# Optimization experiments

Measured on AMD Instinct MI355X. Metric: run time of the kernel, lower is better.

## Reference

```python
import jax, jax.numpy as jnp
import numpy as np
import math

B, S, E = 2, 2048, 1024
H = 16
D = E // H  # head dim = 64


def setup_inputs() -> dict:
    key = jax.random.key(0)
    ks = jax.random.split(key, 9)
    s = 1.0 / math.sqrt(E)
    return {
        "x": jax.random.normal(ks[0], (B, S, E), dtype=jnp.float32),
        "Wq": jax.random.uniform(ks[1], (E, E), jnp.float32, -s, s),
        "bq": jnp.zeros((E,), jnp.float32),
        "Wk": jax.random.uniform(ks[2], (E, E), jnp.float32, -s, s),
        "bk": jnp.zeros((E,), jnp.float32),
        "Wv": jax.random.uniform(ks[3], (E, E), jnp.float32, -s, s),
        "bv": jnp.zeros((E,), jnp.float32),
        "Wo": jax.random.uniform(ks[4], (E, E), jnp.float32, -s, s),
        "bo": jnp.zeros((E,), jnp.float32),
    }


def reference(x, Wq, bq, Wk, bk, Wv, bv, Wo, bo):
    b, s, e = x.shape
    q = x @ Wq + bq  # [B,S,E]
    k = x @ Wk + bk
    v = x @ Wv + bv
    # [B,S,E] -> [B,H,S,D]
    q = q.reshape(b, s, H, D).transpose(0, 2, 1, 3)
    k = k.reshape(b, s, H, D).transpose(0, 2, 1, 3)
    v = v.reshape(b, s, H, D).transpose(0, 2, 1, 3)
    scores = jnp.einsum('bhqd,bhkd->bhqk', q, k) / jnp.sqrt(jnp.float32(D))
    causal = jnp.tril(jnp.ones((s, s), dtype=bool))  # keep lower triangle
    scores = jnp.where(causal, scores, -jnp.inf)
    attn = jax.nn.softmax(scores, axis=-1)
    # dropout is identity in eval mode
    out = jnp.einsum('bhqk,bhkd->bhqd', attn, v)
    out = out.transpose(0, 2, 1, 3).reshape(b, s, e)
    return out @ Wo + bo
```

## Files before the change

kernel.cpp:

```cpp
#include <hip/hip_runtime.h>
#include <hip/hip_bf16.h>
#include <math.h>

#define B_ 2
#define S_ 2048
#define E_ 1024
#define H_ 16
#define D_ 64
#define M_ (B_*S_)

typedef __attribute__((ext_vector_type(8))) short short8v;
typedef __attribute__((ext_vector_type(4))) float floatx4;

__device__ __forceinline__ short f2bf(float f) {
    union { float f; unsigned u; } x; x.f = f;
    unsigned r = (x.u + 0x7fffu + ((x.u >> 16) & 1u)) >> 16;
    return (short)r;
}

__device__ __forceinline__ unsigned pk_bf16(float a, float b) {
    union { float f; unsigned u; } x, y;
    x.f = a; y.f = b;
    return __builtin_amdgcn_perm(y.u + 0x8000u, x.u + 0x8000u, 0x07060302u);
}

__device__ __forceinline__ float fast_exp2(float x) {
#if __has_builtin(__builtin_amdgcn_exp2f)
    return __builtin_amdgcn_exp2f(x);
#else
    return __expf(x * 0.6931471805599453f);
#endif
}

__device__ __forceinline__ void gl2lds16(const void* g, void* l) {
    __builtin_amdgcn_global_load_lds(
        (const __attribute__((address_space(1))) void*)g,
        (__attribute__((address_space(3))) void*)l, 16, 0, 0);
}

__device__ __forceinline__ int swz_off(int row, int cg) {
    return row*64 + (((cg ^ (row & 7)) & 7) << 3);
}

__global__ __launch_bounds__(256) void convert_x(
    const float* __restrict__ x, short* __restrict__ xb)
{
    const size_t i = ((size_t)blockIdx.x*256 + threadIdx.x) * 8;
    float4 a = *(const float4*)(x + i);
    float4 b = *(const float4*)(x + i + 4);
    int4 p = { (int)pk_bf16(a.x,a.y), (int)pk_bf16(a.z,a.w),
               (int)pk_bf16(b.x,b.y), (int)pk_bf16(b.z,b.w) };
    *(int4*)(xb + i) = p;
}

__global__ __launch_bounds__(256) void transpose_w(
    const float* __restrict__ W0, const float* __restrict__ W1,
    const float* __restrict__ W2, const float* __restrict__ W3,
    short* __restrict__ T0, short* __restrict__ T1,
    short* __restrict__ T2, short* __restrict__ T3)
{
    const int z = blockIdx.z;
    const float* W = (z==0)?W0:(z==1)?W1:(z==2)?W2:W3;
    short*       T = (z==0)?T0:(z==1)?T1:(z==2)?T2:T3;
    __shared__ float tile[32][33];
    const int k0 = blockIdx.y*32, n0 = blockIdx.x*32;
    const int r = threadIdx.x >> 5, c = threadIdx.x & 31;
    #pragma unroll
    for (int i=0;i<4;i++)
        tile[r+8*i][c] = W[(size_t)(k0+r+8*i)*E_ + n0 + c];
    __syncthreads();
    #pragma unroll
    for (int i=0;i<4;i++)
        T[(size_t)(n0+r+8*i)*E_ + k0 + c] = f2bf(tile[c][r+8*i]);
}

__global__ __launch_bounds__(512, 2) void qkv_gemm(
    const short* __restrict__ xb, const short* __restrict__ Wt,
    const float* __restrict__ bq, const float* __restrict__ bk, const float* __restrict__ bv,
    short* __restrict__ Qo, short* __restrict__ Ko, short* __restrict__ Vo)
{
    __shared__ __align__(16) short As[2][256*64];
    __shared__ __align__(16) short Bs[2][256*64];

    const int t = threadIdx.x;
    const int wave = t >> 6, lane = t & 63;
    const int quad = lane >> 4, l15 = lane & 15;
    const int wr = wave >> 2, wc = wave & 3;

    const int bid = blockIdx.x;
    const int sw  = (bid & 7) * 24 + (bid >> 3);
    const int m0  = (sw / 12) * 256;
    const int nti = sw % 12;
    const int nf0 = nti * 256;
    const int z   = nf0 >> 10;
    const float* bb = (z==0) ? bq : (z==1) ? bk : bv;
    short* out      = (z==0) ? Qo : (z==1) ? Ko : Vo;
    const float sc  = (z==0) ? 0.18033688011112042f : 1.0f;

    const int sr8 = lane >> 3;
    const int scs = ((lane & 7) ^ sr8) * 8;

    const short* Ag = xb + (size_t)m0  * E_;
    const short* Bg = Wt + (size_t)nf0 * E_;

    floatx4 acc[8][4];
    #pragma unroll
    for (int i=0;i<8;i++)
        #pragma unroll
        for (int j=0;j<4;j++) acc[i][j] = (floatx4){0.f,0.f,0.f,0.f};

    auto stageA = [&](int p, int h, int kt) {
        const int rb = h*128 + wave*16;
        const short* src = Ag + (size_t)(rb + sr8)*E_ + kt*64 + scs;
        #pragma unroll
        for (int c=0;c<2;c++)
            gl2lds16(src + (size_t)c*8*E_, &As[p][(rb + c*8)*64]);
    };
    auto stageB = [&](int p, int h, int kt) {
        const int rb = h*128 + wave*16;
        const short* src = Bg + (size_t)(rb + sr8)*E_ + kt*64 + scs;
        #pragma unroll
        for (int c=0;c<2;c++)
            gl2lds16(src + (size_t)c*8*E_, &Bs[p][(rb + c*8)*64]);
    };

    short8v a[4][2], b[4][2];
    auto rdA = [&](int p, int row16, int ks) -> short8v {
        return *(const short8v*)&As[p][swz_off(wr*128 + row16*16 + l15, quad + ks*4)];
    };
    auto rdB = [&](int p, int row16, int ks) -> short8v {
        return *(const short8v*)&Bs[p][swz_off(wc*64  + row16*16 + l15, quad + ks*4)];
    };
    auto mm = [&](int mbase, int nbase) {
        #pragma unroll
        for (int mt=0;mt<4;mt++)
            #pragma unroll
            for (int nt=0;nt<2;nt++)
                #pragma unroll
                for (int ks=0;ks<2;ks++)
                    acc[mbase+mt][nbase+nt] = __builtin_amdgcn_mfma_f32_16x16x32_bf16(
                        a[mt][ks], b[nbase+nt][ks], acc[mbase+mt][nbase+nt], 0,0,0);
    };

    auto ktile = [&](int tt, int p) {
        #pragma unroll
        for (int mt=0;mt<4;mt++){ a[mt][0]=rdA(p,mt,0); a[mt][1]=rdA(p,mt,1); }
        #pragma unroll
        for (int nt=0;nt<2;nt++){ b[nt][0]=rdB(p,nt,0); b[nt][1]=rdB(p,nt,1); }
        if (tt+1 < 16) stageA(p^1, 0, tt+1);
        __builtin_amdgcn_s_barrier();
        __builtin_amdgcn_s_setprio(1);
        mm(0,0);
        __builtin_amdgcn_s_setprio(0);
        __builtin_amdgcn_s_barrier();
        #pragma unroll
        for (int nt=2;nt<4;nt++){ b[nt][0]=rdB(p,nt,0); b[nt][1]=rdB(p,nt,1); }
        if (tt+1 < 16) stageA(p^1, 1, tt+1);
        __builtin_amdgcn_s_barrier();
        __builtin_amdgcn_s_setprio(1);
        mm(0,2);
        __builtin_amdgcn_s_setprio(0);
        __builtin_amdgcn_s_barrier();
        #pragma unroll
        for (int mt=0;mt<4;mt++){ a[mt][0]=rdA(p,4+mt,0); a[mt][1]=rdA(p,4+mt,1); }
        if (tt+2 < 16) stageB(p, 0, tt+2);
        __builtin_amdgcn_s_barrier();
        __builtin_amdgcn_s_setprio(1);
        mm(4,0);
        __builtin_amdgcn_s_setprio(0);
        __builtin_amdgcn_s_barrier();
        if (tt+2 < 16) stageB(p, 1, tt+2);
        __builtin_amdgcn_s_barrier();
        __builtin_amdgcn_s_setprio(1);
        mm(4,2);
        __builtin_amdgcn_s_setprio(0);
        if (tt+2 < 16)      asm volatile("s_waitcnt vmcnt(4)" ::: "memory");
        else if (tt+1 < 16) asm volatile("s_waitcnt vmcnt(0)" ::: "memory");
        __builtin_amdgcn_s_barrier();
    };

    stageA(0,0,0); stageA(0,1,0); stageB(0,0,0); stageB(0,1,0);
    stageB(1,0,1); stageB(1,1,1);
    asm volatile("s_waitcnt vmcnt(4)" ::: "memory");
    __builtin_amdgcn_s_barrier();

    #pragma unroll 1
    for (int tb = 0; tb < 16; tb += 2) {
        ktile(tb,   0);
        ktile(tb+1, 1);
    }

    #pragma unroll
    for (int nt=0;nt<4;nt++) {
        const int nw = (nf0 & 1023) + wc*64 + nt*16 + l15;
        const float bias = bb[nw];
        const int h = nw >> 6, d = nw & 63;
        #pragma unroll
        for (int mt=0;mt<8;mt++) {
            #pragma unroll
            for (int r=0;r<4;r++) {
                const int m = m0 + wr*128 + mt*16 + quad*4 + r;
                const int b2 = m >> 11, s = m & (S_-1);
                const int bh = (b2<<4) + h;
                const float v = (acc[mt][nt][r] + bias) * sc;
                if (z == 0) {
                    out[((size_t)bh*S_ + s)*D_ + d] = f2bf(v);
                } else if (z == 1) {
                    const int ts = s >> 6, kk = s & 63;
                    const int c = kk*8 + ((d>>3) ^ ((kk>>2)&7));
                    out[((size_t)bh*32 + ts)*4096 + c*8 + (d&7)] = f2bf(v);
                } else {
                    const int ts = s >> 6, sk = s & 63;
                    const int c = d*8 + ((sk>>3) ^ (d&7));
                    out[((size_t)bh*32 + ts)*4096 + c*8 + (sk&7)] = f2bf(v);
                }
            }
        }
    }
}

__global__ __launch_bounds__(256, 1) void attn_kernel(
    const short* __restrict__ Q, const short* __restrict__ K, const short* __restrict__ V,
    short* __restrict__ AO)
{
    const int bh = blockIdx.x;
    const int qb = (gridDim.y - 1 - blockIdx.y) * 128;
    const int t = threadIdx.x;
    const int wave = t >> 6, lane = t & 63;
    const int quad = lane >> 4, l15 = lane & 15;

    const short* Qp = Q + (size_t)bh * (S_*D_);
    const short* Kp = K + (size_t)bh * (S_*D_);
    const short* Vp = V + (size_t)bh * (S_*D_);

    __shared__ __align__(16) short KVs[2][8192];
    __shared__ __align__(16) short Psl[2][4][2][16*72];

    const int qA = qb + wave*16;
    const int qB = qb + 64 + wave*16;
    const short* qa = Qp + (size_t)(qA + l15)*D_ + quad*8;
    const short8v qA0 = *(const short8v*)qa, qA1 = *(const short8v*)(qa + 32);
    const short* qbp = Qp + (size_t)(qB + l15)*D_ + quad*8;
    const short8v qB0 = *(const short8v*)qbp, qB1 = *(const short8v*)(qbp + 32);

    const int qrbA = qA + quad*4;
    const int qrbB = qB + quad*4;

    floatx4 oA[4], oB[4];
    #pragma unroll
    for (int i=0;i<4;i++) { oA[i] = (floatx4){0,0,0,0}; oB[i] = (floatx4){0,0,0,0}; }
    float tsA[4] = {0,0,0,0}, tsB[4] = {0,0,0,0};

    const int L = (qb >> 6) + 2;
    const int swz = l15 & 7;

    auto stage = [&](int kt, int p) {
        const short* src = ((wave < 2) ? Kp : Vp) + (size_t)kt*4096 + (wave&1)*2048 + lane*8;
        short* dst = &KVs[p][((wave < 2) ? 0 : 4096) + (wave&1)*2048];
        #pragma unroll
        for (int c=0;c<4;c++)
            gl2lds16(src + c*512, dst + c*512);
    };
    auto qk2 = [&](const short* KL, floatx4 (&sA)[4], floatx4 (&sB)[4]) {
        #pragma unroll
        for (int h=0; h<4; h++) {
            const int rowc = (4*l15 + h)*8;
            short8v b0 = *(const short8v*)(KL + (rowc + (quad       ^ swz))*8);
            short8v b1 = *(const short8v*)(KL + (rowc + ((4 + quad) ^ swz))*8);
            sA[h] = (floatx4){0.f,0.f,0.f,0.f};
            sA[h] = __builtin_amdgcn_mfma_f32_16x16x32_bf16(qA0, b0, sA[h], 0,0,0);
            sA[h] = __builtin_amdgcn_mfma_f32_16x16x32_bf16(qA1, b1, sA[h], 0,0,0);
            sB[h] = (floatx4){0.f,0.f,0.f,0.f};
            sB[h] = __builtin_amdgcn_mfma_f32_16x16x32_bf16(qB0, b0, sB[h], 0,0,0);
            sB[h] = __builtin_amdgcn_mfma_f32_16x16x32_bf16(qB1, b1, sB[h], 0,0,0);
        }
    };
    auto soft_u = [&](floatx4 (&s)[4], float* ts, short* pw, int qrb, int k0) {
        const int kk = k0 + 4*l15;
        #pragma unroll
        for (int r=0; r<4; r++) {
            const int qr = qrb + r;
            float p[4];
            #pragma unroll
            for (int h=0; h<4; h++) {
                const float e = fast_exp2(s[h][r]);
                p[h] = (kk + h > qr) ? 0.f : e;
            }
            ts[r] += (p[0] + p[1]) + (p[2] + p[3]);
            int2 pkv = { (int)pk_bf16(p[0], p[1]), (int)pk_bf16(p[2], p[3]) };
            *(int2*)(pw + (quad*4 + r)*72 + l15*4) = pkv;
        }
    };
    short8v vr[4][2];
    auto loadv = [&](const short* VL) {
        #pragma unroll
        for (int dt=0; dt<4; dt++) {
            const int rowc = (dt*16 + l15)*8;
            vr[dt][0] = *(const short8v*)(VL + (rowc + (quad       ^ swz))*8);
            vr[dt][1] = *(const short8v*)(VL + (rowc + ((4 + quad) ^ swz))*8);
        }
    };
    auto pv = [&](const short* pw, floatx4 (&o)[4]) {
        const short8v pf0 = *(const short8v*)(pw + l15*72 + quad*8);
        const short8v pf1 = *(const short8v*)(pw + l15*72 + 32 + quad*8);
        #pragma unroll
        for (int dt=0; dt<4; dt++) {
            o[dt] = __builtin_amdgcn_mfma_f32_16x16x32_bf16(pf0, vr[dt][0], o[dt], 0,0,0);
            o[dt] = __builtin_amdgcn_mfma_f32_16x16x32_bf16(pf1, vr[dt][1], o[dt], 0,0,0);
        }
    };

    stage(0, 0);
    __syncthreads();
    stage(1, 1);
    {
        floatx4 sA[4], sB[4];
        qk2(&KVs[0][0], sA, sB);
        loadv(&KVs[0][4096]);
        soft_u(sA, tsA, &Psl[0][wave][0][0], qrbA, 0);
        soft_u(sB, tsB, &Psl[0][wave][1][0], qrbB, 0);
    }

    for (int kt = 1; kt < L; kt++) {
        const int p = kt & 1;
        __syncthreads();
        if (kt + 1 < L) stage(kt + 1, p ^ 1);
        floatx4 sA[4], sB[4];
        qk2(&KVs[p][0], sA, sB);
        pv(&Psl[p^1][wave][0][0], oA);
        pv(&Psl[p^1][wave][1][0], oB);
        loadv(&KVs[p][4096]);
        const int k0 = kt << 6;
        soft_u(sA, tsA, &Psl[p][wave][0][0], qrbA, k0);
        soft_u(sB, tsB, &Psl[p][wave][1][0], qrbB, k0);
    }

    pv(&Psl[1][wave][0][0], oA);
    pv(&Psl[1][wave][1][0], oB);

    float lA[4], lB[4];
    #pragma unroll
    for (int r=0; r<4; r++) {
        float a = tsA[r], b = tsB[r];
        #pragma unroll
        for (int off=1; off<16; off<<=1) {
            a += __shfl_xor(a, off);
            b += __shfl_xor(b, off);
        }
        lA[r] = a; lB[r] = b;
    }

    const int b = bh >> 4, h = bh & 15;
    #pragma unroll
    for (int dt=0; dt<4; dt++) {
        #pragma unroll
        for (int r=0; r<4; r++) {
            const int d = dt*16 + l15;
            const int sA_ = qA + quad*4 + r;
            const int sB_ = qB + quad*4 + r;
            AO[((size_t)(b*S_ + sA_)*H_ + h)*D_ + d] = f2bf(oA[dt][r] / lA[r]);
            AO[((size_t)(b*S_ + sB_)*H_ + h)*D_ + d] = f2bf(oB[dt][r] / lB[r]);
        }
    }
}

__global__ __launch_bounds__(256) void out_gemm(
    const short* __restrict__ A, const short* __restrict__ Wto,
    const float* __restrict__ bo, float* __restrict__ out)
{
    __shared__ __align__(16) short As[128*64];
    __shared__ __align__(16) short Bs[64*64];

    const int t = threadIdx.x;
    const int wave = t >> 6, lane = t & 63;
    const int quad = lane >> 4, l15 = lane & 15;
    const int lin = blockIdx.x;
    const int m0 = (lin & 31) * 128;
    const int n0 = (lin >> 5) * 64;
    const int sr8 = lane >> 3;
    const int scs = ((lane & 7) ^ sr8) * 8;

    floatx4 acc[2][4];
    #pragma unroll
    for (int i=0;i<2;i++)
        #pragma unroll
        for (int j=0;j<4;j++) acc[i][j] = (floatx4){0.f,0.f,0.f,0.f};

    for (int k0 = 0; k0 < E_; k0 += 64) {
        #pragma unroll
        for (int c=0;c<4;c++) {
            const int rb = wave*32 + c*8;
            gl2lds16(A + (size_t)(m0+rb+sr8)*E_ + k0 + scs, &As[rb*64]);
        }
        #pragma unroll
        for (int c=0;c<2;c++) {
            const int rb = wave*16 + c*8;
            gl2lds16(Wto + (size_t)(n0+rb+sr8)*E_ + k0 + scs, &Bs[rb*64]);
        }
        __syncthreads();
        #pragma unroll
        for (int ks=0; ks<2; ks++) {
            const int cg = quad + ks*4;
            short8v a[2], b[4];
            #pragma unroll
            for (int mt=0;mt<2;mt++) a[mt] = *(const short8v*)&As[swz_off(wave*32+mt*16+l15, cg)];
            #pragma unroll
            for (int nt=0;nt<4;nt++) b[nt] = *(const short8v*)&Bs[swz_off(nt*16+l15, cg)];
            #pragma unroll
            for (int mt=0;mt<2;mt++)
                #pragma unroll
                for (int nt=0;nt<4;nt++)
                    acc[mt][nt] = __builtin_amdgcn_mfma_f32_16x16x32_bf16(a[mt], b[nt], acc[mt][nt], 0,0,0);
        }
        __syncthreads();
    }

    #pragma unroll
    for (int nt=0;nt<4;nt++) {
        const int n = n0 + nt*16 + l15;
        const float bias = bo[n];
        #pragma unroll
        for (int mt=0;mt<2;mt++) {
            #pragma unroll
            for (int r=0;r<4;r++) {
                const int m = m0 + wave*32 + mt*16 + quad*4 + r;
                out[(size_t)m*E_ + n] = acc[mt][nt][r] + bias;
            }
        }
    }
}

extern "C" void kernel_launch(void* const* d_in, const int* in_sizes, int n_in,
                              void* d_out, int out_size, void* d_ws, size_t ws_size,
                              hipStream_t stream)
{
    const float* x  = (const float*)d_in[0];
    const float* Wq = (const float*)d_in[1];
    const float* bq = (const float*)d_in[2];
    const float* Wk = (const float*)d_in[3];
    const float* bk = (const float*)d_in[4];
    const float* Wv = (const float*)d_in[5];
    const float* bv = (const float*)d_in[6];
    const float* Wo = (const float*)d_in[7];
    const float* bo = (const float*)d_in[8];

    short* xb  = (short*)d_ws;
    short* Tq  = xb  + (size_t)M_ * E_;
    short* Tk  = Tq  + (size_t)E_ * E_;
    short* Tv  = Tk  + (size_t)E_ * E_;
    short* To  = Tv  + (size_t)E_ * E_;
    short* Qw  = To  + (size_t)E_ * E_;
    short* Kw  = Qw  + (size_t)M_ * E_;
    short* Vw  = Kw  + (size_t)M_ * E_;
    short* AOw = Vw  + (size_t)M_ * E_;

    dim3 blk(256);
    convert_x<<<dim3((M_*E_)/(256*8)), blk, 0, stream>>>(x, xb);
    transpose_w<<<dim3(E_/32, E_/32, 4), blk, 0, stream>>>(Wq, Wk, Wv, Wo, Tq, Tk, Tv, To);
    qkv_gemm<<<dim3(192), dim3(512), 0, stream>>>(xb, Tq, bq, bk, bv, Qw, Kw, Vw);
    attn_kernel<<<dim3(B_*H_, S_/128), blk, 0, stream>>>(Qw, Kw, Vw, AOw);
    out_gemm<<<dim3(512), blk, 0, stream>>>(AOw, To, bo, (float*)d_out);
}
```

Measured before the change: 195.5 us.

## Fuse prep kernels, stage QKV epilogue through LDS, add MFMA priority hints

Merges the x conversion and weight transpose into one launch to cut a kernel launch. The QKV GEMM epilogue now writes tiles to a reused LDS buffer and then issues 16-byte vectorized global stores in place of scattered 2-byte stores, including a transposed path for V. Attention QK and PV MFMA blocks get s_setprio hints, and the B/A fragment load order is swapped. The LDS reuse relies on the main loop's final barrier before the buffer is overwritten.

```diff
diff --git a/kernel.cpp b/kernel.cpp
--- a/kernel.cpp
+++ b/kernel.cpp
@@ -42,28 +42,29 @@
     return row*64 + (((cg ^ (row & 7)) & 7) << 3);
 }
 
-__global__ __launch_bounds__(256) void convert_x(
-    const float* __restrict__ x, short* __restrict__ xb)
-{
-    const size_t i = ((size_t)blockIdx.x*256 + threadIdx.x) * 8;
-    float4 a = *(const float4*)(x + i);
-    float4 b = *(const float4*)(x + i + 4);
-    int4 p = { (int)pk_bf16(a.x,a.y), (int)pk_bf16(a.z,a.w),
-               (int)pk_bf16(b.x,b.y), (int)pk_bf16(b.z,b.w) };
-    *(int4*)(xb + i) = p;
-}
-
-__global__ __launch_bounds__(256) void transpose_w(
+__global__ __launch_bounds__(256) void prep(
+    const float* __restrict__ x, short* __restrict__ xb,
     const float* __restrict__ W0, const float* __restrict__ W1,
     const float* __restrict__ W2, const float* __restrict__ W3,
     short* __restrict__ T0, short* __restrict__ T1,
     short* __restrict__ T2, short* __restrict__ T3)
 {
-    const int z = blockIdx.z;
+    const int bid = blockIdx.x;
+    if (bid < 2048) {
+        const size_t i = ((size_t)bid*256 + threadIdx.x) * 8;
+        float4 a = *(const float4*)(x + i);
+        float4 b = *(const float4*)(x + i + 4);
+        int4 p = { (int)pk_bf16(a.x,a.y), (int)pk_bf16(a.z,a.w),
+                   (int)pk_bf16(b.x,b.y), (int)pk_bf16(b.z,b.w) };
+        *(int4*)(xb + i) = p;
+        return;
+    }
+    const int tb = bid - 2048;
+    const int z = tb >> 10;
     const float* W = (z==0)?W0:(z==1)?W1:(z==2)?W2:W3;
     short*       T = (z==0)?T0:(z==1)?T1:(z==2)?T2:T3;
     __shared__ float tile[32][33];
-    const int k0 = blockIdx.y*32, n0 = blockIdx.x*32;
+    const int k0 = ((tb>>5)&31)*32, n0 = (tb&31)*32;
     const int r = threadIdx.x >> 5, c = threadIdx.x & 31;
     #pragma unroll
     for (int i=0;i<4;i++)
@@ -79,8 +80,9 @@
     const float* __restrict__ bq, const float* __restrict__ bk, const float* __restrict__ bv,
     short* __restrict__ Qo, short* __restrict__ Ko, short* __restrict__ Vo)
 {
-    __shared__ __align__(16) short As[2][256*64];
-    __shared__ __align__(16) short Bs[2][256*64];
+    __shared__ __align__(16) short SMEM[65536];
+    short* Asp = SMEM;
+    short* Bsp = SMEM + 32768;
 
     const int t = threadIdx.x;
     const int wave = t >> 6, lane = t & 63;
@@ -114,22 +116,22 @@
         const short* src = Ag + (size_t)(rb + sr8)*E_ + kt*64 + scs;
         #pragma unroll
         for (int c=0;c<2;c++)
-            gl2lds16(src + (size_t)c*8*E_, &As[p][(rb + c*8)*64]);
+            gl2lds16(src + (size_t)c*8*E_, Asp + p*16384 + (rb + c*8)*64);
     };
     auto stageB = [&](int p, int h, int kt) {
         const int rb = h*128 + wave*16;
         const short* src = Bg + (size_t)(rb + sr8)*E_ + kt*64 + scs;
         #pragma unroll
         for (int c=0;c<2;c++)
-            gl2lds16(src + (size_t)c*8*E_, &Bs[p][(rb + c*8)*64]);
+            gl2lds16(src + (size_t)c*8*E_, Bsp + p*16384 + (rb + c*8)*64);
     };
 
     short8v a[4][2], b[4][2];
     auto rdA = [&](int p, int row16, int ks) -> short8v {
-        return *(const short8v*)&As[p][swz_off(wr*128 + row16*16 + l15, quad + ks*4)];
+        return *(const short8v*)&Asp[p*16384 + swz_off(wr*128 + row16*16 + l15, quad + ks*4)];
     };
     auto rdB = [&](int p, int row16, int ks) -> short8v {
-        return *(const short8v*)&Bs[p][swz_off(wc*64  + row16*16 + l15, quad + ks*4)];
+        return *(const short8v*)&Bsp[p*16384 + swz_off(wc*64  + row16*16 + l15, quad + ks*4)];
     };
     auto mm = [&](int mbase, int nbase) {
         #pragma unroll
@@ -144,9 +146,9 @@
 
     auto ktile = [&](int tt, int p) {
         #pragma unroll
+        for (int nt=0;nt<2;nt++){ b[nt][0]=rdB(p,nt,0); b[nt][1]=rdB(p,nt,1); }
+        #pragma unroll
         for (int mt=0;mt<4;mt++){ a[mt][0]=rdA(p,mt,0); a[mt][1]=rdA(p,mt,1); }
-        #pragma unroll
-        for (int nt=0;nt<2;nt++){ b[nt][0]=rdB(p,nt,0); b[nt][1]=rdB(p,nt,1); }
         if (tt+1 < 16) stageA(p^1, 0, tt+1);
         __builtin_amdgcn_s_barrier();
         __builtin_amdgcn_s_setprio(1);
@@ -190,31 +192,67 @@
         ktile(tb+1, 1);
     }
 
-    #pragma unroll
-    for (int nt=0;nt<4;nt++) {
-        const int nw = (nf0 & 1023) + wc*64 + nt*16 + l15;
-        const float bias = bb[nw];
-        const int h = nw >> 6, d = nw & 63;
-        #pragma unroll
-        for (int mt=0;mt<8;mt++) {
-            #pragma unroll
-            for (int r=0;r<4;r++) {
-                const int m = m0 + wr*128 + mt*16 + quad*4 + r;
-                const int b2 = m >> 11, s = m & (S_-1);
-                const int bh = (b2<<4) + h;
-                const float v = (acc[mt][nt][r] + bias) * sc;
-                if (z == 0) {
-                    out[((size_t)bh*S_ + s)*D_ + d] = f2bf(v);
-                } else if (z == 1) {
-                    const int ts = s >> 6, kk = s & 63;
-                    const int c = kk*8 + ((d>>3) ^ ((kk>>2)&7));
-                    out[((size_t)bh*32 + ts)*4096 + c*8 + (d&7)] = f2bf(v);
-                } else {
-                    const int ts = s >> 6, sk = s & 63;
-                    const int c = d*8 + ((sk>>3) ^ (d&7));
-                    out[((size_t)bh*32 + ts)*4096 + c*8 + (sk&7)] = f2bf(v);
+    short* wbuf = SMEM + wave*8192;
+    const int nwbase = (nf0 & 1023) + wc*64;
+    const int h = nwbase >> 6;
+    const int mbase = m0 + wr*128;
+    const int bh = ((mbase >> 11) << 4) + h;
+
+    if (z != 2) {
+        #pragma unroll
+        for (int nt=0;nt<4;nt++) {
+            const int c = nt*16 + l15;
+            const float bias = bb[nwbase + c];
+            #pragma unroll
+            for (int mt=0;mt<8;mt++)
+                #pragma unroll
+                for (int r=0;r<4;r++) {
+                    const int rr = mt*16 + quad*4 + r;
+                    wbuf[rr*64 + (((c>>3) ^ (rr&7)) << 3) + (c&7)] =
+                        f2bf((acc[mt][nt][r] + bias) * sc);
                 }
+        }
+        asm volatile("s_waitcnt lgkmcnt(0)" ::: "memory");
+        __builtin_amdgcn_sched_barrier(0);
+        #pragma unroll
+        for (int it=0; it<16; it++) {
+            const int rr = it*8 + (lane>>3);
+            const int cg = lane & 7;
+            short8v v = *(const short8v*)&wbuf[rr*64 + ((cg ^ (rr&7)) << 3)];
+            const int s = (mbase + rr) & (S_-1);
+            if (z == 0) {
+                *(short8v*)&out[((size_t)bh*S_ + s)*D_ + cg*8] = v;
+            } else {
+                const int ts = s >> 6, kk = s & 63;
+                const int csw = kk*8 + (cg ^ ((kk>>2)&7));
+                *(short8v*)&out[((size_t)bh*32 + ts)*4096 + csw*8] = v;
             }
+        }
+    } else {
+        #pragma unroll
+        for (int nt=0;nt<4;nt++) {
+            const int d = nt*16 + l15;
+            const float bias = bb[nwbase + d];
+            #pragma unroll
+            for (int mt=0;mt<8;mt++)
+                #pragma unroll
+                for (int r=0;r<4;r++) {
+                    const int sl = mt*16 + quad*4 + r;
+                    wbuf[d*128 + (((sl>>3) ^ (d&15)) << 3) + (sl&7)] =
+                        f2bf(acc[mt][nt][r] + bias);
+                }
+        }
+        asm volatile("s_waitcnt lgkmcnt(0)" ::: "memory");
+        __builtin_amdgcn_sched_barrier(0);
+        #pragma unroll
+        for (int it=0; it<16; it++) {
+            const int d  = (it&7)*8 + (lane>>3);
+            const int cg = (it>>3)*8 + (lane&7);
+            short8v v = *(const short8v*)&wbuf[d*128 + ((cg ^ (d&15)) << 3)];
+            const int sb = (mbase & (S_-1)) + cg*8;
+            const int ts = sb >> 6;
+            const int csw = d*8 + (((sb>>3)&7) ^ (d&7));
+            *(short8v*)&out[((size_t)bh*32 + ts)*4096 + csw*8] = v;
         }
     }
 }
@@ -262,6 +300,7 @@
             gl2lds16(src + c*512, dst + c*512);
     };
     auto qk2 = [&](const short* KL, floatx4 (&sA)[4], floatx4 (&sB)[4]) {
+        __builtin_amdgcn_s_setprio(1);
         #pragma unroll
         for (int h=0; h<4; h++) {
             const int rowc = (4*l15 + h)*8;
@@ -274,6 +313,7 @@
             sB[h] = __builtin_amdgcn_mfma_f32_16x16x32_bf16(qB0, b0, sB[h], 0,0,0);
             sB[h] = __builtin_amdgcn_mfma_f32_16x16x32_bf16(qB1, b1, sB[h], 0,0,0);
         }
+        __builtin_amdgcn_s_setprio(0);
     };
     auto soft_u = [&](floatx4 (&s)[4], float* ts, short* pw, int qrb, int k0) {
         const int kk = k0 + 4*l15;
@@ -303,11 +343,13 @@
     auto pv = [&](const short* pw, floatx4 (&o)[4]) {
         const short8v pf0 = *(const short8v*)(pw + l15*72 + quad*8);
         const short8v pf1 = *(const short8v*)(pw + l15*72 + 32 + quad*8);
+        __builtin_amdgcn_s_setprio(1);
         #pragma unroll
         for (int dt=0; dt<4; dt++) {
             o[dt] = __builtin_amdgcn_mfma_f32_16x16x32_bf16(pf0, vr[dt][0], o[dt], 0,0,0);
             o[dt] = __builtin_amdgcn_mfma_f32_16x16x32_bf16(pf1, vr[dt][1], o[dt], 0,0,0);
         }
+        __builtin_amdgcn_s_setprio(0);
     };
 
     stage(0, 0);
@@ -455,8 +497,7 @@
     short* AOw = Vw  + (size_t)M_ * E_;
 
     dim3 blk(256);
-    convert_x<<<dim3((M_*E_)/(256*8)), blk, 0, stream>>>(x, xb);
-    transpose_w<<<dim3(E_/32, E_/32, 4), blk, 0, stream>>>(Wq, Wk, Wv, Wo, Tq, Tk, Tv, To);
+    prep<<<dim3(2048 + 4096), blk, 0, stream>>>(x, xb, Wq, Wk, Wv, Wo, Tq, Tk, Tv, To);
     qkv_gemm<<<dim3(192), dim3(512), 0, stream>>>(xb, Tq, bq, bk, bv, Qw, Kw, Vw);
     attn_kernel<<<dim3(B_*H_, S_/128), blk, 0, stream>>>(Qw, Kw, Vw, AOw);
     out_gemm<<<dim3(512), blk, 0, stream>>>(AOw, To, bo, (float*)d_out);
```

New measurement: 184.2 us. 1.06x faster.
